# Kernel tuning notes

Measured on AMD Instinct MI355X. Metric: run time of the kernel, lower is better.

Reference implementation:

```python
import jax, jax.numpy as jnp
import numpy as np

NUM_HEADS = 12
H = W = 64            # spatial grid (SAM ViT-B global attention)
DIM = 768
HEAD_DIM = DIM // NUM_HEADS


def setup_inputs() -> dict:
    key = jax.random.key(0)
    ks = jax.random.split(key, 7)
    return {
        "x": jax.random.normal(ks[0], (1, H, W, DIM), dtype=jnp.float32),
        "qkv_w": jax.random.normal(ks[1], (3 * DIM, DIM), dtype=jnp.float32) * 0.02,
        "qkv_b": jax.random.normal(ks[2], (3 * DIM,), dtype=jnp.float32) * 0.02,
        "proj_w": jax.random.normal(ks[3], (DIM, DIM), dtype=jnp.float32) * 0.02,
        "proj_b": jax.random.normal(ks[4], (DIM,), dtype=jnp.float32) * 0.02,
        "rel_pos_h": jax.random.normal(ks[5], (2 * H - 1, HEAD_DIM), dtype=jnp.float32) * 0.02,
        "rel_pos_w": jax.random.normal(ks[6], (2 * W - 1, HEAD_DIM), dtype=jnp.float32) * 0.02,
    }


def _get_rel_pos(size: int, rel_pos: jnp.ndarray) -> jnp.ndarray:
    # q_size == k_size == size; rel_pos already has length 2*size-1 (no interp).
    coords = jnp.arange(size)[:, None] - jnp.arange(size)[None, :] + (size - 1)
    return rel_pos[coords]  # [size, size, head_dim]


def reference(x, qkv_w, qkv_b, proj_w, proj_b, rel_pos_h, rel_pos_w):
    B, h, w, C = x.shape
    nh, hd = NUM_HEADS, C // NUM_HEADS
    S = h * w
    scale = hd ** -0.5

    qkv = x.reshape(B, S, C) @ qkv_w.T + qkv_b            # [B, S, 3C]
    qkv = qkv.reshape(B, S, 3, nh, hd).transpose(2, 0, 3, 1, 4)
    qkv = qkv.reshape(3, B * nh, S, hd)
    q, k, v = qkv[0], qkv[1], qkv[2]                      # [B*nh, S, hd]

    attn = jnp.einsum('bqc,bkc->bqk', q * scale, k)       # [B*nh, S, S]

    Rh = _get_rel_pos(h, rel_pos_h)                       # [h, h, hd]
    Rw = _get_rel_pos(w, rel_pos_w)                       # [w, w, hd]
    r_q = q.reshape(B * nh, h, w, hd)
    rel_h = jnp.einsum('bhwc,hkc->bhwk', r_q, Rh)         # [B*nh, h, w, h]
    rel_w = jnp.einsum('bhwc,wkc->bhwk', r_q, Rw)         # [B*nh, h, w, w]
    attn = (attn.reshape(B * nh, h, w, h, w)
            + rel_h[:, :, :, :, None]
            + rel_w[:, :, :, None, :]).reshape(B * nh, S, S)

    attn = jax.nn.softmax(attn, axis=-1)
    out = jnp.einsum('bqk,bkc->bqc', attn, v)             # [B*nh, S, hd]
    out = out.reshape(B, nh, h, w, hd).transpose(0, 2, 3, 1, 4).reshape(B, h, w, C)
    return out @ proj_w.T + proj_b
```

## Files before the change

### kernel.cpp

```cpp
#include <hip/hip_runtime.h>


typedef __bf16 bf16;
typedef __bf16 bf16x8 __attribute__((ext_vector_type(8)));
typedef __bf16 bf16x4 __attribute__((ext_vector_type(4)));
typedef float f32x4 __attribute__((ext_vector_type(4)));
typedef float f32x16 __attribute__((ext_vector_type(16)));
typedef unsigned int u32;

__device__ __forceinline__ f32x4 mfma16(bf16x8 a, bf16x8 b, f32x4 c) {
  return __builtin_amdgcn_mfma_f32_16x16x32_bf16(a, b, c, 0, 0, 0);
}
__device__ __forceinline__ f32x16 mfma32(bf16x8 a, bf16x8 b, f32x16 c) {
  return __builtin_amdgcn_mfma_f32_32x32x16_bf16(a, b, c, 0, 0, 0);
}

typedef const __attribute__((address_space(1))) void* gas_ptr;
typedef __attribute__((address_space(3))) void* las_ptr;
__device__ __forceinline__ void gl_lds16(const void* g, void* l) {
  __builtin_amdgcn_global_load_lds((gas_ptr)g, (las_ptr)l, 16, 0, 0);
}

#if defined(__has_builtin)
#if __has_builtin(__builtin_amdgcn_permlane32_swap)
#define HAVE_PLSWAP 1
#endif
#endif
__device__ __forceinline__ void pswap_u(u32& a, u32& b) {
#ifdef HAVE_PLSWAP
  auto r = __builtin_amdgcn_permlane32_swap(a, b, false, false);
  a = r[0]; b = r[1];
#else
  const bool hi = (threadIdx.x & 32) != 0;
  u32 sa = (u32)__shfl_xor((int)a, 32, 64);
  u32 sb = (u32)__shfl_xor((int)b, 32, 64);
  u32 na = hi ? sb : a;
  u32 nb = hi ? b : sa;
  a = na; b = nb;
#endif
}
__device__ __forceinline__ void pswap_f(float& a, float& b) {
  u32 x = __float_as_uint(a), y = __float_as_uint(b);
  pswap_u(x, y);
  a = __uint_as_float(x); b = __uint_as_float(y);
}

#define L2E 1.4426950408889634f

__global__ __launch_bounds__(256) void cvt3(
    const float* __restrict__ a, bf16* __restrict__ oa,
    const float* __restrict__ b, bf16* __restrict__ ob,
    const float* __restrict__ c, bf16* __restrict__ oc) {
  int blk = blockIdx.x;
  const float* src;
  bf16* dst;
  int base;
  if (blk < 1536)       { src = a; dst = oa; base = blk; }
  else if (blk < 2400)  { src = b; dst = ob; base = blk - 1536; }
  else                  { src = c; dst = oc; base = blk - 2400; }
  int idx = (base * 256 + threadIdx.x) * 8;
  f32x4 x = *(const f32x4*)&src[idx];
  f32x4 y = *(const f32x4*)&src[idx + 4];
  bf16x8 o;
#pragma unroll
  for (int j = 0; j < 4; j++) { o[j] = (bf16)x[j]; o[j + 4] = (bf16)y[j]; }
  *(bf16x8*)&dst[idx] = o;
}

template <int MODE>
__global__ __launch_bounds__(256) void gemm128(
    const bf16* __restrict__ A, const bf16* __restrict__ B,
    const float* __restrict__ bias, int K, int N,
    bf16* __restrict__ q_s, bf16* __restrict__ k_s, bf16* __restrict__ v_t,
    float* __restrict__ outf) {
  __shared__ __align__(16) bf16 lA[128 * 64];
  __shared__ __align__(16) bf16 lB[128 * 64];
  const int tid = threadIdx.x;
  const int w = tid >> 6, l = tid & 63;
  const int n0 = blockIdx.x * 128, m0 = blockIdx.y * 128;

  f32x4 acc[4][4] = {};

  int rowc[4], sloc[4];
#pragma unroll
  for (int j = 0; j < 4; j++) {
    const int c = w * 4 + j;
    rowc[j] = c * 8 + (l >> 3);
    sloc[j] = (((l & 7) ^ (l >> 3) ^ c) & 7) * 8;
  }
  const int mw = (w & 1) * 64, nw = (w >> 1) * 64;

  for (int k0 = 0; k0 < K; k0 += 64) {
    __syncthreads();
#pragma unroll
    for (int j = 0; j < 4; j++) {
      gl_lds16(&A[(size_t)(m0 + rowc[j]) * K + k0 + sloc[j]],
               (char*)lA + (w * 4 + j) * 1024);
      gl_lds16(&B[(size_t)(n0 + rowc[j]) * K + k0 + sloc[j]],
               (char*)lB + (w * 4 + j) * 1024);
    }
    __syncthreads();
    bf16x8 af[2][4], bfr[2][4];
#pragma unroll
    for (int ks = 0; ks < 2; ks++)
#pragma unroll
      for (int i = 0; i < 4; i++) {
        const int rA = mw + i * 16 + (l & 15);
        const int rB = nw + i * 16 + (l & 15);
        const int slot = ks * 4 + (l >> 4);
        const int fA = ((rA ^ (rA >> 3)) & 7), fB = ((rB ^ (rB >> 3)) & 7);
        af[ks][i] = *(const bf16x8*)((const char*)lA + rA * 128 + ((slot ^ fA) & 7) * 16);
        bfr[ks][i] = *(const bf16x8*)((const char*)lB + rB * 128 + ((slot ^ fB) & 7) * 16);
      }
#pragma unroll
    for (int ks = 0; ks < 2; ks++)
#pragma unroll
      for (int mi = 0; mi < 4; mi++)
#pragma unroll
        for (int ni = 0; ni < 4; ni++)
          acc[mi][ni] = mfma16(af[ks][mi], bfr[ks][ni], acc[mi][ni]);
  }

  if (MODE == 0 && n0 >= 1536) {
    bf16* Lt = lA;
#pragma unroll 1
    for (int pass = 0; pass < 2; ++pass) {
      __syncthreads();
      if ((w >> 1) == pass) {
        char* R = (char*)Lt + (w & 1) * 8192;
#pragma unroll
        for (int ni = 0; ni < 4; ni++) {
          const float bv = bias[n0 + nw + ni * 16 + (l & 15)];
          const int nl = ni * 16 + (l & 15);
#pragma unroll
          for (int mi = 0; mi < 4; mi++)
#pragma unroll
            for (int i2 = 0; i2 < 2; i2++) {
              const int ml2 = (mi * 16 + (l >> 4) * 4 + i2 * 2) * 2;
              union { bf16 b[2]; u32 u; } pk;
              pk.b[0] = (bf16)(acc[mi][ni][i2 * 2] + bv);
              pk.b[1] = (bf16)(acc[mi][ni][i2 * 2 + 1] + bv);
              *(u32*)(R + nl * 128 + (ml2 ^ ((nl & 7) << 4))) = pk.u;
            }
        }
      }
      __syncthreads();
      if ((w >> 1) == pass) {
        const char* R = (const char*)Lt + (w & 1) * 8192;
#pragma unroll
        for (int r = 0; r < 8; r++) {
          const int nl = r * 8 + (l >> 3);
          const int pc = ((l & 7) * 16) ^ ((nl & 7) << 4);
          bf16x8 val = *(const bf16x8*)(R + nl * 128 + pc);
          const int n = n0 + pass * 64 + nl;
          const int head = (n - 1536) >> 6, hd = n & 63;
          *(bf16x8*)&v_t[((size_t)(head * 64 + hd)) * 4096 + m0 + (w & 1) * 64 +
                         (l & 7) * 8] = val;
        }
      }
    }
    return;
  }

#pragma unroll
  for (int ni = 0; ni < 4; ni++) {
    const int n = n0 + nw + ni * 16 + (l & 15);
    const float bv = bias[n];
#pragma unroll
    for (int mi = 0; mi < 4; mi++) {
#pragma unroll
      for (int i = 0; i < 4; i++) {
        const int m = m0 + mw + mi * 16 + (l >> 4) * 4 + i;
        const float v = acc[mi][ni][i] + bv;
        if (MODE == 0) {
          const int which = n / 768, hn = n % 768;
          const int head = hn >> 6, hd = hn & 63;
          if (which == 0)      q_s[((size_t)head * 4096 + m) * 64 + hd] = (bf16)v;
          else                 k_s[((size_t)head * 4096 + m) * 64 + hd] = (bf16)v;
        } else {
          outf[(size_t)m * N + n] = v;
        }
      }
    }
  }
}

__global__ __launch_bounds__(64) void rel_pos_w(
    const bf16* __restrict__ q_s, const float* __restrict__ table,
    float* __restrict__ out) {
  const int l = threadIdx.x;
  const int p = blockIdx.x, head = blockIdx.y;
  const size_t hbase = (size_t)head * 4096 * 64;

  f32x4 acc[4][4] = {};
#pragma unroll
  for (int ks = 0; ks < 2; ks++) {
    bf16x8 af[4], bfr[4];
#pragma unroll
    for (int mi = 0; mi < 4; mi++) {
      const int row = mi * 16 + (l & 15);
      const int s = row * 64 + p;
      af[mi] = *(const bf16x8*)&q_s[hbase + (size_t)s * 64 + ks * 32 + (l >> 4) * 8];
    }
#pragma unroll
    for (int ni = 0; ni < 4; ni++) {
      const int col = ni * 16 + (l & 15);
      const float* tp = &table[(size_t)(p - col + 63) * 64 + ks * 32 + (l >> 4) * 8];
      f32x4 t0 = *(const f32x4*)tp;
      f32x4 t1 = *(const f32x4*)(tp + 4);
      bf16x8 bb;
#pragma unroll
      for (int j = 0; j < 4; j++) { bb[j] = (bf16)t0[j]; bb[j + 4] = (bf16)t1[j]; }
      bfr[ni] = bb;
    }
#pragma unroll
    for (int mi = 0; mi < 4; mi++)
#pragma unroll
      for (int ni = 0; ni < 4; ni++)
        acc[mi][ni] = mfma16(af[mi], bfr[ni], acc[mi][ni]);
  }
#pragma unroll
  for (int mi = 0; mi < 4; mi++)
#pragma unroll
    for (int ni = 0; ni < 4; ni++)
#pragma unroll
      for (int i = 0; i < 4; i++) {
        const int row = mi * 16 + (l >> 4) * 4 + i;
        const int col = ni * 16 + (l & 15);
        const int sq = row * 64 + p;
        out[hbase + (size_t)sq * 64 + col] = acc[mi][ni][i];
      }
}

__global__ __launch_bounds__(256) void flash_attn(
    const bf16* __restrict__ q_s, const bf16* __restrict__ k_s,
    const bf16* __restrict__ v_t, const float* __restrict__ rph,
    const float* __restrict__ bias_w, bf16* __restrict__ attn_out) {
  __shared__ __align__(16) char smem[49408];
  float* lBH = (float*)(smem + 32768);

  const int tid = threadIdx.x;
  const int w = tid >> 6, l = tid & 63;
  const int r5 = l & 31, h = l >> 5;
  const int qg = w & 1, kh2 = w >> 1;
  const int f = blockIdx.x;
  const int g = (f & 7) * 96 + (f >> 3);
  const int head = g >> 6, qh = g & 63;
  const size_t hbase = (size_t)head << 18;
  const int qloc = qg * 32 + r5;
  const size_t sq = (size_t)qh * 64 + qloc;

  const int ch0 = w * 2, ch1 = ch0 + 1;
  const int lr3 = l >> 3;
  const int swz0 = (((l & 7) ^ lr3 ^ ch0) & 7) * 8;
  const int swz1 = (((l & 7) ^ lr3 ^ ch1) & 7) * 8;
  const bf16* kp0 = k_s + hbase + (size_t)(ch0 * 8 + lr3) * 64 + swz0;
  const bf16* kp1 = k_s + hbase + (size_t)(ch1 * 8 + lr3) * 64 + swz1;
  const bf16* vp0 = v_t + hbase + (size_t)(ch0 * 8 + lr3) * 4096 + swz0;
  const bf16* vp1 = v_t + hbase + (size_t)(ch1 * 8 + lr3) * 4096 + swz1;

#define STAGE(buf)                                                        \
  do {                                                                    \
    gl_lds16(kp0, smem + (buf) * 8192 + ch0 * 1024);                      \
    gl_lds16(kp1, smem + (buf) * 8192 + ch1 * 1024);                      \
    gl_lds16(vp0, smem + 16384 + (buf) * 8192 + ch0 * 1024);              \
    gl_lds16(vp1, smem + 16384 + (buf) * 8192 + ch1 * 1024);              \
  } while (0)

  STAGE(0);
  kp0 += 4096; kp1 += 4096; vp0 += 64; vp1 += 64;

  {
    const int q16 = l & 15, g4 = l >> 4;
    const size_t sq16 = (size_t)qh * 64 + w * 16 + q16;
    bf16x8 qf16[2];
    qf16[0] = *(const bf16x8*)&q_s[hbase + sq16 * 64 + g4 * 8];
    qf16[1] = *(const bf16x8*)&q_s[hbase + sq16 * 64 + 32 + g4 * 8];
    f32x4 abh[4] = {};
#pragma unroll
    for (int ks = 0; ks < 2; ks++)
#pragma unroll
      for (int ni = 0; ni < 4; ni++) {
        const int kh = ni * 16 + q16;
        const float* tp = &rph[(size_t)(qh + 63 - kh) * 64 + ks * 32 + g4 * 8];
        f32x4 t0 = *(const f32x4*)tp;
        f32x4 t1 = *(const f32x4*)(tp + 4);
        bf16x8 rf;
#pragma unroll
        for (int j = 0; j < 4; j++) { rf[j] = (bf16)t0[j]; rf[j + 4] = (bf16)t1[j]; }
        abh[ni] = mfma16(rf, qf16[ks], abh[ni]);
      }
#pragma unroll
    for (int ni = 0; ni < 4; ni++)
#pragma unroll
      for (int i = 0; i < 4; i++)
        lBH[(w * 16 + q16) * 65 + ni * 16 + g4 * 4 + i] = abh[ni][i];
  }

  bf16x8 qv[4];
#pragma unroll
  for (int s = 0; s < 4; s++)
    qv[s] = *(const bf16x8*)&q_s[hbase + sq * 64 + s * 16 + h * 8];

  float c2[16];
#pragma unroll
  for (int G = 0; G < 4; G++) {
    f32x4 cv = *(const f32x4*)&bias_w[hbase + sq * 64 + kh2 * 32 + G * 8 + h * 4];
#pragma unroll
    for (int i = 0; i < 4; i++) c2[G * 4 + i] = cv[i] * L2E;
  }

  int offK[4], offV[2][2];
  const int rowK = kh2 * 32 + r5;
  const int fK = ((l & 7) ^ (kh2 * 4 + ((l >> 3) & 3))) & 7;
#pragma unroll
  for (int s = 0; s < 4; s++)
    offK[s] = rowK * 128 + (((s * 2 + h) ^ fK) & 7) * 16;
#pragma unroll
  for (int T = 0; T < 2; T++) {
    const int fV = ((l & 7) ^ (T * 4 + ((l >> 3) & 3))) & 7;
#pragma unroll
    for (int st = 0; st < 2; st++)
      offV[T][st] = (T * 32 + r5) * 128 + (((kh2 * 4 + st * 2 + h) ^ fV) & 7) * 16;
  }

  f32x16 o[2] = {};
  float mrun = -1e30f, lrun = 0.f;
  const float SC2 = 0.125f * L2E;

  auto compute = [&](int t) {
    const char* kb = smem + (t & 1) * 8192;
    const char* vb = smem + 16384 + (t & 1) * 8192;

    f32x16 sacc = {0.f, 0.f, 0.f, 0.f, 0.f, 0.f, 0.f, 0.f,
                   0.f, 0.f, 0.f, 0.f, 0.f, 0.f, 0.f, 0.f};
    __builtin_amdgcn_s_setprio(1);
#pragma unroll
    for (int s = 0; s < 4; s++) {
      bf16x8 kf = *(const bf16x8*)(kb + offK[s]);
      sacc = mfma32(kf, qv[s], sacc);
    }
    __builtin_amdgcn_s_setprio(0);

    float p[16], pm = -1e30f;
#pragma unroll
    for (int j = 0; j < 16; j++) {
      p[j] = sacc[j] * SC2 + c2[j];
      pm = fmaxf(pm, p[j]);
    }
    { float t2 = pm; pswap_f(t2, pm); pm = fmaxf(t2, pm); }
    const float bh2 = lBH[qloc * 65 + t] * L2E;
    const float rmf = pm + bh2;

    if (!__all(rmf - mrun <= 8.f)) {
      const float mn = fmaxf(mrun, rmf);
      const float al = __builtin_amdgcn_exp2f(mrun - mn);
      mrun = mn;
      lrun *= al;
      o[0] *= al;
      o[1] *= al;
    }

    const float d = bh2 - mrun;
    float rs = 0.f;
    u32 w8[8];
#pragma unroll
    for (int j = 0; j < 8; j++) {
      float e0 = __builtin_amdgcn_exp2f(p[2 * j] + d);
      float e1 = __builtin_amdgcn_exp2f(p[2 * j + 1] + d);
      rs += e0 + e1;
      union { bf16 b[2]; u32 u; } cvu;
      cvu.b[0] = (bf16)e0;
      cvu.b[1] = (bf16)e1;
      w8[j] = cvu.u;
    }
    { float t2 = rs; pswap_f(t2, rs); rs = t2 + rs; }
    lrun += rs;

#pragma unroll
    for (int st = 0; st < 2; st++) {
      union { u32 u[4]; bf16x8 v; } pf;
      u32 a0 = w8[4 * st], b0 = w8[4 * st + 2];
      u32 a1 = w8[4 * st + 1], b1 = w8[4 * st + 3];
      pswap_u(a0, b0);
      pswap_u(a1, b1);
      pf.u[0] = a0; pf.u[1] = a1; pf.u[2] = b0; pf.u[3] = b1;
      __builtin_amdgcn_s_setprio(1);
#pragma unroll
      for (int T = 0; T < 2; T++) {
        bf16x8 vf = *(const bf16x8*)(vb + offV[T][st]);
        o[T] = mfma32(vf, pf.v, o[T]);
      }
      __builtin_amdgcn_s_setprio(0);
    }
  };

  __syncthreads();

  for (int t = 0; t < 63; t++) {
    STAGE((t + 1) & 1);
    kp0 += 4096; kp1 += 4096; vp0 += 64; vp1 += 64;
    asm volatile("s_waitcnt vmcnt(4)" ::: "memory");
    __builtin_amdgcn_s_barrier();
    __builtin_amdgcn_sched_barrier(0);
    compute(t);
    __builtin_amdgcn_s_barrier();
    __builtin_amdgcn_sched_barrier(0);
  }
  asm volatile("s_waitcnt vmcnt(0)" ::: "memory");
  __builtin_amdgcn_s_barrier();
  __builtin_amdgcn_sched_barrier(0);
  compute(63);
  __syncthreads();

  float* MM = (float*)smem;
  float* ML = (float*)(smem + 256);
  float* MO = (float*)(smem + 512);
  if (w >= 2) {
    if (h == 0) { MM[qg * 32 + r5] = mrun; ML[qg * 32 + r5] = lrun; }
#pragma unroll
    for (int T = 0; T < 2; T++)
#pragma unroll
      for (int G = 0; G < 4; G++) {
        f32x4 ov;
#pragma unroll
        for (int i = 0; i < 4; i++) ov[i] = o[T][4 * G + i];
        *(f32x4*)&MO[qg * 2048 + r5 * 64 + T * 32 + G * 8 + h * 4] = ov;
      }
  }
  __syncthreads();
  if (w < 2) {
    const float mp = MM[qg * 32 + r5], lp = ML[qg * 32 + r5];
    const float mT = fmaxf(mrun, mp);
    const float a = __builtin_amdgcn_exp2f(mrun - mT);
    const float b = __builtin_amdgcn_exp2f(mp - mT);
    const float inv = 1.f / (lrun * a + lp * b);
#pragma unroll
    for (int T = 0; T < 2; T++)
#pragma unroll
      for (int G = 0; G < 4; G++) {
        f32x4 po = *(const f32x4*)&MO[qg * 2048 + r5 * 64 + T * 32 + G * 8 + h * 4];
        bf16x4 ob;
#pragma unroll
        for (int i = 0; i < 4; i++)
          ob[i] = (bf16)((o[T][4 * G + i] * a + po[i] * b) * inv);
        *(bf16x4*)&attn_out[sq * 768 + head * 64 + T * 32 + G * 8 + h * 4] = ob;
      }
  }
#undef STAGE
}

extern "C" void kernel_launch(void* const* d_in, const int* in_sizes, int n_in,
                              void* d_out, int out_size, void* d_ws, size_t ws_size,
                              hipStream_t stream) {
  const float* x      = (const float*)d_in[0];
  const float* qkv_w  = (const float*)d_in[1];
  const float* qkv_b  = (const float*)d_in[2];
  const float* proj_w = (const float*)d_in[3];
  const float* proj_b = (const float*)d_in[4];
  const float* rph    = (const float*)d_in[5];
  const float* rpw    = (const float*)d_in[6];

  char* ws = (char*)d_ws;
  bf16*  xb    = (bf16*)(ws);
  bf16*  wqkv  = (bf16*)(ws + 6291456);
  bf16*  wproj = (bf16*)(ws + 9830400);
  bf16*  q_s   = (bf16*)(ws + 11010048);
  bf16*  k_s   = (bf16*)(ws + 17301504);
  bf16*  v_t   = (bf16*)(ws + 23592960);
  bf16*  attno = (bf16*)(ws + 29884416);
  float* bwv   = (float*)(ws + 36175872);

  cvt3<<<2688, 256, 0, stream>>>(x, xb, qkv_w, wqkv, proj_w, wproj);

  gemm128<0><<<dim3(18, 32), 256, 0, stream>>>(xb, wqkv, qkv_b, 768, 2304,
                                               q_s, k_s, v_t, nullptr);

  rel_pos_w<<<dim3(64, 12), 64, 0, stream>>>(q_s, rpw, bwv);

  flash_attn<<<768, 256, 0, stream>>>(q_s, k_s, v_t, rph, bwv, attno);

  gemm128<1><<<dim3(6, 32), 256, 0, stream>>>(attno, wproj, proj_b, 768, 768,
                                              nullptr, nullptr, nullptr,
                                              (float*)d_out);
}
```

Before: 241.7 us.

## Pre-swizzle K/V into MFMA fragment layout and load directly from global

The QKV GEMM epilogue now writes K (prescaled by scale*log2e) and V in the exact per-lane fragment order the attention MFMAs consume. The flash kernel then drops its LDS double-buffered staging and barriers, reading K/V fragments straight from global/L2. It also seeds the score accumulator with the rel-w bias, pre-multiplies the rel-h bias by log2e, shrinks LDS, and asks for 3 waves per SIMD. The GEMM also remaps its block order for locality. The cost is that each wave issues its own global loads and latency is no longer hidden by the explicit pipeline, though higher occupancy may cover it.

```diff
diff --git a/kernel.cpp b/kernel.cpp
--- a/kernel.cpp
+++ b/kernel.cpp
@@ -46,6 +46,7 @@
 }
 
 #define L2E 1.4426950408889634f
+#define SCK 0.18033688011112042f
 
 __global__ __launch_bounds__(256) void cvt3(
     const float* __restrict__ a, bf16* __restrict__ oa,
@@ -71,13 +72,17 @@
 __global__ __launch_bounds__(256) void gemm128(
     const bf16* __restrict__ A, const bf16* __restrict__ B,
     const float* __restrict__ bias, int K, int N,
-    bf16* __restrict__ q_s, bf16* __restrict__ k_s, bf16* __restrict__ v_t,
+    bf16* __restrict__ q_s, bf16* __restrict__ k_f, bf16* __restrict__ v_f,
     float* __restrict__ outf) {
   __shared__ __align__(16) bf16 lA[128 * 64];
   __shared__ __align__(16) bf16 lB[128 * 64];
   const int tid = threadIdx.x;
   const int w = tid >> 6, l = tid & 63;
-  const int n0 = blockIdx.x * 128, m0 = blockIdx.y * 128;
+  const int nbx = gridDim.x;
+  const int flat = blockIdx.y * nbx + blockIdx.x;
+  const int nwg = nbx * gridDim.y;
+  const int idx = (flat & 7) * (nwg >> 3) + (flat >> 3);
+  const int n0 = (idx % nbx) * 128, m0 = (idx / nbx) * 128;
 
   f32x4 acc[4][4] = {};
 
@@ -154,8 +159,13 @@
           bf16x8 val = *(const bf16x8*)(R + nl * 128 + pc);
           const int n = n0 + pass * 64 + nl;
           const int head = (n - 1536) >> 6, hd = n & 63;
-          *(bf16x8*)&v_t[((size_t)(head * 64 + hd)) * 4096 + m0 + (w & 1) * 64 +
-                         (l & 7) * 8] = val;
+          const int mg = m0 + (w & 1) * 64 + (l & 7) * 8;
+          const int t = mg >> 6, kh2 = (mg >> 5) & 1;
+          const int st = (mg >> 4) & 1, hh = (mg >> 3) & 1;
+          const size_t vidx =
+              ((((((size_t)head * 64 + t) * 2 + kh2) * 2 + st) * 2 + hh) * 64 +
+               hd) * 8;
+          *(bf16x8*)&v_f[vidx] = val;
         }
       }
     }
@@ -175,8 +185,16 @@
         if (MODE == 0) {
           const int which = n / 768, hn = n % 768;
           const int head = hn >> 6, hd = hn & 63;
-          if (which == 0)      q_s[((size_t)head * 4096 + m) * 64 + hd] = (bf16)v;
-          else                 k_s[((size_t)head * 4096 + m) * 64 + hd] = (bf16)v;
+          if (which == 0) {
+            q_s[((size_t)head * 4096 + m) * 64 + hd] = (bf16)v;
+          } else {
+            const int t = m >> 6, kh2 = (m >> 5) & 1, r5 = m & 31;
+            const int s = hd >> 4, h = (hd >> 3) & 1, j = hd & 7;
+            const size_t kidx =
+                ((((((size_t)head * 64 + t) * 2 + kh2) * 4 + s) * 2 + h) * 32 +
+                 r5) * 8 + j;
+            k_f[kidx] = (bf16)(v * SCK);
+          }
         } else {
           outf[(size_t)m * N + n] = v;
         }
@@ -232,12 +250,12 @@
       }
 }
 
-__global__ __launch_bounds__(256) void flash_attn(
-    const bf16* __restrict__ q_s, const bf16* __restrict__ k_s,
-    const bf16* __restrict__ v_t, const float* __restrict__ rph,
+__global__ __launch_bounds__(256, 3) void flash_attn(
+    const bf16* __restrict__ q_s, const bf16* __restrict__ k_f,
+    const bf16* __restrict__ v_f, const float* __restrict__ rph,
     const float* __restrict__ bias_w, bf16* __restrict__ attn_out) {
-  __shared__ __align__(16) char smem[49408];
-  float* lBH = (float*)(smem + 32768);
+  __shared__ __align__(16) char smem[16896];
+  float* lBH = (float*)smem;
 
   const int tid = threadIdx.x;
   const int w = tid >> 6, l = tid & 63;
@@ -250,26 +268,6 @@
   const int qloc = qg * 32 + r5;
   const size_t sq = (size_t)qh * 64 + qloc;
 
-  const int ch0 = w * 2, ch1 = ch0 + 1;
-  const int lr3 = l >> 3;
-  const int swz0 = (((l & 7) ^ lr3 ^ ch0) & 7) * 8;
-  const int swz1 = (((l & 7) ^ lr3 ^ ch1) & 7) * 8;
-  const bf16* kp0 = k_s + hbase + (size_t)(ch0 * 8 + lr3) * 64 + swz0;
-  const bf16* kp1 = k_s + hbase + (size_t)(ch1 * 8 + lr3) * 64 + swz1;
-  const bf16* vp0 = v_t + hbase + (size_t)(ch0 * 8 + lr3) * 4096 + swz0;
-  const bf16* vp1 = v_t + hbase + (size_t)(ch1 * 8 + lr3) * 4096 + swz1;
-
-#define STAGE(buf)                                                        \
-  do {                                                                    \
-    gl_lds16(kp0, smem + (buf) * 8192 + ch0 * 1024);                      \
-    gl_lds16(kp1, smem + (buf) * 8192 + ch1 * 1024);                      \
-    gl_lds16(vp0, smem + 16384 + (buf) * 8192 + ch0 * 1024);              \
-    gl_lds16(vp1, smem + 16384 + (buf) * 8192 + ch1 * 1024);              \
-  } while (0)
-
-  STAGE(0);
-  kp0 += 4096; kp1 += 4096; vp0 += 64; vp1 += 64;
-
   {
     const int q16 = l & 15, g4 = l >> 4;
     const size_t sq16 = (size_t)qh * 64 + w * 16 + q16;
@@ -294,7 +292,7 @@
     for (int ni = 0; ni < 4; ni++)
 #pragma unroll
       for (int i = 0; i < 4; i++)
-        lBH[(w * 16 + q16) * 65 + ni * 16 + g4 * 4 + i] = abh[ni][i];
+        lBH[(w * 16 + q16) * 65 + ni * 16 + g4 * 4 + i] = abh[ni][i] * L2E;
   }
 
   bf16x8 qv[4];
@@ -302,54 +300,41 @@
   for (int s = 0; s < 4; s++)
     qv[s] = *(const bf16x8*)&q_s[hbase + sq * 64 + s * 16 + h * 8];
 
-  float c2[16];
+  f32x16 c2v;
 #pragma unroll
   for (int G = 0; G < 4; G++) {
     f32x4 cv = *(const f32x4*)&bias_w[hbase + sq * 64 + kh2 * 32 + G * 8 + h * 4];
 #pragma unroll
-    for (int i = 0; i < 4; i++) c2[G * 4 + i] = cv[i] * L2E;
-  }
-
-  int offK[4], offV[2][2];
-  const int rowK = kh2 * 32 + r5;
-  const int fK = ((l & 7) ^ (kh2 * 4 + ((l >> 3) & 3))) & 7;
-#pragma unroll
-  for (int s = 0; s < 4; s++)
-    offK[s] = rowK * 128 + (((s * 2 + h) ^ fK) & 7) * 16;
-#pragma unroll
-  for (int T = 0; T < 2; T++) {
-    const int fV = ((l & 7) ^ (T * 4 + ((l >> 3) & 3))) & 7;
-#pragma unroll
-    for (int st = 0; st < 2; st++)
-      offV[T][st] = (T * 32 + r5) * 128 + (((kh2 * 4 + st * 2 + h) ^ fV) & 7) * 16;
-  }
+    for (int i = 0; i < 4; i++) c2v[G * 4 + i] = cv[i] * L2E;
+  }
+
+  const bf16* kp = k_f + hbase + kh2 * 2048 + h * 256 + r5 * 8;
+  const bf16* vp = v_f + hbase + kh2 * 2048 + h * 512 + r5 * 8;
+  const float* lbhp = lBH + qloc * 65;
 
   f32x16 o[2] = {};
   float mrun = -1e30f, lrun = 0.f;
-  const float SC2 = 0.125f * L2E;
-
-  auto compute = [&](int t) {
-    const char* kb = smem + (t & 1) * 8192;
-    const char* vb = smem + 16384 + (t & 1) * 8192;
-
-    f32x16 sacc = {0.f, 0.f, 0.f, 0.f, 0.f, 0.f, 0.f, 0.f,
-                   0.f, 0.f, 0.f, 0.f, 0.f, 0.f, 0.f, 0.f};
+
+  __syncthreads();
+
+  for (int t = 0; t < 64; t++) {
+    f32x16 sacc = c2v;
     __builtin_amdgcn_s_setprio(1);
 #pragma unroll
     for (int s = 0; s < 4; s++) {
-      bf16x8 kf = *(const bf16x8*)(kb + offK[s]);
+      bf16x8 kf = *(const bf16x8*)((const char*)kp + s * 1024);
       sacc = mfma32(kf, qv[s], sacc);
     }
     __builtin_amdgcn_s_setprio(0);
 
-    float p[16], pm = -1e30f;
-#pragma unroll
-    for (int j = 0; j < 16; j++) {
-      p[j] = sacc[j] * SC2 + c2[j];
-      pm = fmaxf(pm, p[j]);
-    }
+    float pm = fmaxf(
+        fmaxf(fmaxf(fmaxf(sacc[0], sacc[1]), sacc[2]),
+              fmaxf(fmaxf(sacc[3], sacc[4]), sacc[5])),
+        fmaxf(fmaxf(fmaxf(sacc[6], sacc[7]), fmaxf(sacc[8], sacc[9])),
+              fmaxf(fmaxf(sacc[10], fmaxf(sacc[11], sacc[12])),
+                    fmaxf(sacc[13], fmaxf(sacc[14], sacc[15])))));
     { float t2 = pm; pswap_f(t2, pm); pm = fmaxf(t2, pm); }
-    const float bh2 = lBH[qloc * 65 + t] * L2E;
+    const float bh2 = lbhp[t];
     const float rmf = pm + bh2;
 
     if (!__all(rmf - mrun <= 8.f)) {
@@ -366,8 +351,8 @@
     u32 w8[8];
 #pragma unroll
     for (int j = 0; j < 8; j++) {
-      float e0 = __builtin_amdgcn_exp2f(p[2 * j] + d);
-      float e1 = __builtin_amdgcn_exp2f(p[2 * j + 1] + d);
+      float e0 = __builtin_amdgcn_exp2f(sacc[2 * j] + d);
+      float e1 = __builtin_amdgcn_exp2f(sacc[2 * j + 1] + d);
       rs += e0 + e1;
       union { bf16 b[2]; u32 u; } cvu;
       cvu.b[0] = (bf16)e0;
@@ -388,29 +373,16 @@
       __builtin_amdgcn_s_setprio(1);
 #pragma unroll
       for (int T = 0; T < 2; T++) {
-        bf16x8 vf = *(const bf16x8*)(vb + offV[T][st]);
+        bf16x8 vf = *(const bf16x8*)((const char*)vp + st * 2048 + T * 512);
         o[T] = mfma32(vf, pf.v, o[T]);
       }
       __builtin_amdgcn_s_setprio(0);
     }
-  };
-
-  __syncthreads();
-
-  for (int t = 0; t < 63; t++) {
-    STAGE((t + 1) & 1);
-    kp0 += 4096; kp1 += 4096; vp0 += 64; vp1 += 64;
-    asm volatile("s_waitcnt vmcnt(4)" ::: "memory");
-    __builtin_amdgcn_s_barrier();
-    __builtin_amdgcn_sched_barrier(0);
-    compute(t);
-    __builtin_amdgcn_s_barrier();
-    __builtin_amdgcn_sched_barrier(0);
-  }
-  asm volatile("s_waitcnt vmcnt(0)" ::: "memory");
-  __builtin_amdgcn_s_barrier();
-  __builtin_amdgcn_sched_barrier(0);
-  compute(63);
+
+    kp += 4096;
+    vp += 4096;
+  }
+
   __syncthreads();
 
   float* MM = (float*)smem;
@@ -447,7 +419,6 @@
         *(bf16x4*)&attn_out[sq * 768 + head * 64 + T * 32 + G * 8 + h * 4] = ob;
       }
   }
-#undef STAGE
 }
 
 extern "C" void kernel_launch(void* const* d_in, const int* in_sizes, int n_in,
@@ -466,19 +437,19 @@
   bf16*  wqkv  = (bf16*)(ws + 6291456);
   bf16*  wproj = (bf16*)(ws + 9830400);
   bf16*  q_s   = (bf16*)(ws + 11010048);
-  bf16*  k_s   = (bf16*)(ws + 17301504);
-  bf16*  v_t   = (bf16*)(ws + 23592960);
+  bf16*  k_f   = (bf16*)(ws + 17301504);
+  bf16*  v_f   = (bf16*)(ws + 23592960);
   bf16*  attno = (bf16*)(ws + 29884416);
   float* bwv   = (float*)(ws + 36175872);
 
   cvt3<<<2688, 256, 0, stream>>>(x, xb, qkv_w, wqkv, proj_w, wproj);
 
   gemm128<0><<<dim3(18, 32), 256, 0, stream>>>(xb, wqkv, qkv_b, 768, 2304,
-                                               q_s, k_s, v_t, nullptr);
+                                               q_s, k_f, v_f, nullptr);
 
   rel_pos_w<<<dim3(64, 12), 64, 0, stream>>>(q_s, rpw, bwv);
 
-  flash_attn<<<768, 256, 0, stream>>>(q_s, k_s, v_t, rph, bwv, attno);
+  flash_attn<<<768, 256, 0, stream>>>(q_s, k_f, v_f, rph, bwv, attno);
 
   gemm128<1><<<dim3(6, 32), 256, 0, stream>>>(attno, wproj, proj_b, 768, 768,
                                               nullptr, nullptr, nullptr,
```

New measurement: 257.3 us. 1.06x slower.
